# Kernel tuning notes

Measured on AMD Instinct MI355X. Metric: run time of the kernel, lower is better.

## Reference

```python
import jax, jax.numpy as jnp
import numpy as np

B, NPG, CIN, D, C, H, E, MAXN = 128, 1000, 16, 128, 12, 4, 640000, 1001
N = B * NPG
DH = D // H
NL = 3


def _ln(x, w, b):
    m = x.mean(-1, keepdims=True)
    v = ((x - m) ** 2).mean(-1, keepdims=True)
    return (x - m) * jax.lax.rsqrt(v + 1e-5) * w + b


def _mha(q_in, k_in, v_in, qkv_w, qkv_b, out_w, out_b, pad=None):
    # torch nn.MultiheadAttention with packed in_proj: rows [0:D]=Q, [D:2D]=K, [2D:3D]=V
    Tq, Tk = q_in.shape[1], k_in.shape[1]
    q = (q_in @ qkv_w[:D].T + qkv_b[:D]).reshape(-1, Tq, H, DH)
    k = (k_in @ qkv_w[D:2 * D].T + qkv_b[D:2 * D]).reshape(-1, Tk, H, DH)
    v = (v_in @ qkv_w[2 * D:].T + qkv_b[2 * D:]).reshape(-1, Tk, H, DH)
    s = jnp.einsum('bqhd,bkhd->bhqk', q, k) / np.sqrt(DH).astype(np.float32)
    if pad is not None:
        s = jnp.where(pad[:, None, None, :], jnp.float32(-1e30), s)
    a = jax.nn.softmax(s, axis=-1)
    o = jnp.einsum('bhqk,bkhd->bqhd', a, v).reshape(-1, Tq, D)
    return o @ out_w.T + out_b


def setup_inputs():
    key = jax.random.key(0)
    ks = iter(jax.random.split(key, 48))
    def nrm(shape, s=0.05):
        return jax.random.normal(next(ks), shape, jnp.float32) * s
    inp = {
        'x': nrm((N, CIN), 1.0),
        'edge_index': jax.random.randint(next(ks), (2, E), 0, N, dtype=jnp.int32),
        'batch': (jnp.arange(N, dtype=jnp.int32) // NPG),
        'in_w': nrm((D, CIN)), 'in_b': nrm((D,)),
        'gcn_w': nrm((NL, D, D)), 'gcn_b': nrm((NL, D)),
        'ln_w': jnp.ones((NL, D), jnp.float32), 'ln_b': jnp.zeros((NL, D), jnp.float32),
        'cq': nrm((C, D), 1.0),
        'sa_qkv_w': nrm((3 * D, D)), 'sa_qkv_b': nrm((3 * D,)),
        'sa_out_w': nrm((D, D)), 'sa_out_b': nrm((D,)),
        'ca_qkv_w': nrm((3 * D, D)), 'ca_qkv_b': nrm((3 * D,)),
        'ca_out_w': nrm((D, D)), 'ca_out_b': nrm((D,)),
        'n1_w': jnp.ones((D,), jnp.float32), 'n1_b': jnp.zeros((D,), jnp.float32),
        'n2_w': jnp.ones((D,), jnp.float32), 'n2_b': jnp.zeros((D,), jnp.float32),
        'n3_w': jnp.ones((D,), jnp.float32), 'n3_b': jnp.zeros((D,), jnp.float32),
        'ff1_w': nrm((4 * D, D)), 'ff1_b': nrm((4 * D,)),
        'ff2_w': nrm((D, 4 * D)), 'ff2_b': nrm((D,)),
        'op_ln_w': jnp.ones((D,), jnp.float32), 'op_ln_b': jnp.zeros((D,), jnp.float32),
        'op_w': nrm((1, D)), 'op_b': nrm((1,)),
    }
    return inp


def reference(x, edge_index, batch, in_w, in_b, gcn_w, gcn_b, ln_w, ln_b, cq,
              sa_qkv_w, sa_qkv_b, sa_out_w, sa_out_b,
              ca_qkv_w, ca_qkv_b, ca_out_w, ca_out_b,
              n1_w, n1_b, n2_w, n2_b, n3_w, n3_b,
              ff1_w, ff1_b, ff2_w, ff2_b, op_ln_w, op_ln_b, op_w, op_b):
    row, col = edge_index[0], edge_index[1]
    # ---- GCNBlock (eval mode: dropout = identity) ----
    h = x @ in_w.T + in_b  # input_proj since in_channels != hidden_dim
    # GCNConv normalization with self-loops (same for all layers)
    deg = jax.ops.segment_sum(jnp.ones((E,), h.dtype), col, num_segments=N) + 1.0
    dinv = jax.lax.rsqrt(deg)  # [N]
    en = dinv[row] * dinv[col]  # [E]
    self_w = (dinv * dinv)[:, None]
    residual = h
    for i in range(NL):
        hw = h @ gcn_w[i].T  # [N, D]
        agg = jax.ops.segment_sum(en[:, None] * hw[row], col, num_segments=N)
        agg = agg + self_w * hw + gcn_b[i]
        if i < NL - 1:
            h = jax.nn.relu(_ln(agg, ln_w[i], ln_b[i]))
            h = h + residual
            residual = h
        else:
            h = _ln(agg, ln_w[i], ln_b[i])
    # ---- pad variable-size graphs into dense memory + key padding mask ----
    counts = jax.ops.segment_sum(jnp.ones((N,), jnp.int32), batch, num_segments=B)
    starts = jnp.cumsum(counts) - counts
    pos = jnp.arange(N, dtype=jnp.int32) - starts[batch]
    memory = jnp.zeros((B, MAXN, D), h.dtype).at[batch, pos].set(h)
    pad = jnp.arange(MAXN)[None, :] >= counts[:, None]  # True = padded position
    # ---- TransformerDecoderLayer (norm_first=True), 1 layer ----
    t = jnp.broadcast_to(cq, (B, C, D))
    tn = _ln(t, n1_w, n1_b)
    t = t + _mha(tn, tn, tn, sa_qkv_w, sa_qkv_b, sa_out_w, sa_out_b)
    tn = _ln(t, n2_w, n2_b)
    t = t + _mha(tn, memory, memory, ca_qkv_w, ca_qkv_b, ca_out_w, ca_out_b, pad)
    tn = _ln(t, n3_w, n3_b)
    t = t + (jax.nn.relu(tn @ ff1_w.T + ff1_b) @ ff2_w.T + ff2_b)
    # ---- output projection: LN -> Linear(D,1) -> squeeze ----
    logits = (_ln(t, op_ln_w, op_ln_b) @ op_w.T + op_b)[..., 0]  # [B, C]
    return logits
```

## Files before the change

### kernel.cpp

```cpp
#include <hip/hip_runtime.h>
#include <hip/hip_bf16.h>

#define NNODES 128000
#define NEDGES 640000
#define BB 128
#define CC 12
#define DD 128
#define NROWS (BB*CC)
#define NSPLIT 8
#define CHUNK 125

typedef __attribute__((ext_vector_type(8))) short short8;
typedef __attribute__((ext_vector_type(4))) float f32x4;
typedef unsigned short ushort_t;

__device__ __forceinline__ unsigned pk2bf(float lo, float hi){
    union { __hip_bfloat162 h; unsigned u; } v;
    v.h = __float22bfloat162_rn(make_float2(lo, hi));
    return v.u;
}
__device__ __forceinline__ ushort_t f2bf(float f){
    union { __hip_bfloat16 h; ushort_t u; } v;
    v.h = __float2bfloat16(f);
    return v.u;
}
__device__ __forceinline__ float bfu_lo(unsigned u){
    union { unsigned u; float f; } v; v.u = u << 16; return v.f;
}
__device__ __forceinline__ float bfu_hi(unsigned u){
    union { unsigned u; float f; } v; v.u = u & 0xFFFF0000u; return v.f;
}

__global__ __launch_bounds__(256) void count_edges(const int* __restrict__ col, int* __restrict__ cnt){
    int e = blockIdx.x*256 + threadIdx.x;
    if (e < NEDGES) atomicAdd(&cnt[col[e]], 1);
}

__global__ __launch_bounds__(256) void scan_a(const int* __restrict__ cnt, int* __restrict__ offs,
        int* __restrict__ bsum, float* __restrict__ dinv){
    __shared__ int tmp[256];
    int tid = threadIdx.x;
    int g = blockIdx.x*256 + tid;
    int v = cnt[g];
    dinv[g] = rsqrtf((float)v + 1.0f);
    tmp[tid] = v;
    __syncthreads();
    for (int o=1;o<256;o<<=1){
        int a = (tid>=o)? tmp[tid-o] : 0;
        __syncthreads();
        tmp[tid] += a;
        __syncthreads();
    }
    offs[g] = tmp[tid] - v;
    if (tid==255) bsum[blockIdx.x] = tmp[255];
}

__global__ __launch_bounds__(512) void scan_b(int* __restrict__ bsum, int NB){
    __shared__ int tmp[512];
    int tid = threadIdx.x;
    int v = (tid<NB)? bsum[tid] : 0;
    tmp[tid] = v;
    __syncthreads();
    for (int o=1;o<512;o<<=1){
        int a = (tid>=o)? tmp[tid-o] : 0;
        __syncthreads();
        tmp[tid] += a;
        __syncthreads();
    }
    if (tid<NB) bsum[tid] = tmp[tid] - v;
}

__global__ __launch_bounds__(256) void scan_c(int* __restrict__ offs, const int* __restrict__ bsum){
    int g = blockIdx.x*256 + threadIdx.x;
    offs[g] += bsum[g>>8];
    if (g==0) offs[NNODES] = NEDGES;
}

__global__ __launch_bounds__(256) void fill_csr(const int* __restrict__ row, const int* __restrict__ col,
        const int* __restrict__ offs, int* __restrict__ cur, const float* __restrict__ dinv,
        int2* __restrict__ ee){
    int e = blockIdx.x*256 + threadIdx.x;
    if (e >= NEDGES) return;
    int c = col[e], r = row[e];
    int p = atomicAdd(&cur[c], 1);
    int idx = offs[c] + p;
    float w = dinv[r]*dinv[c];
    ee[idx] = make_int2(r, __float_as_int(w));
}

__global__ __launch_bounds__(256) void conv_all(const float* __restrict__ gcn_w,
        const float* __restrict__ ca_qkv_w, const float* __restrict__ in_w,
        const float* __restrict__ caout, const float* __restrict__ ff1, const float* __restrict__ ff2,
        ushort_t* __restrict__ Wb, ushort_t* __restrict__ Wpad, ushort_t* __restrict__ Wd){
    int i = blockIdx.x*256 + threadIdx.x;
    if (i < 81920){
        int slot = i >> 14, off = i & 16383;
        float v = (slot < 3) ? gcn_w[slot*16384 + off]
                             : ca_qkv_w[16384 + (slot-3)*16384 + off];
        Wb[i] = f2bf(v);
    } else if (i < 86016){
        int j = i - 81920;
        int n = j >> 5, k = j & 31;
        Wpad[j] = (k < 16) ? f2bf(in_w[n*16 + k]) : (ushort_t)0;
    } else {
        int j = i - 86016;
        float v;
        if (j < 16384) v = caout[j];
        else if (j < 81920) v = ff1[j - 16384];
        else v = ff2[j - 81920];
        Wd[j] = f2bf(v);
    }
}

__global__ __launch_bounds__(256) void in_proj_mfma(const float* __restrict__ x,
        const ushort_t* __restrict__ Wpad, const float* __restrict__ bias,
        ushort_t* __restrict__ hbf){
    __shared__ __align__(16) ushort_t xs[64*40];
    int tid = threadIdx.x;
    int m0 = blockIdx.x*64;
    if (tid < 128){
        short8 z = {0,0,0,0,0,0,0,0};
        *(short8*)&xs[(tid>>1)*40 + 16 + (tid&1)*8] = z;
    }
    float4 xv = *(const float4*)(x + (size_t)m0*16 + tid*4);
    uint2 pk2;
    pk2.x = pk2bf(xv.x, xv.y);
    pk2.y = pk2bf(xv.z, xv.w);
    *(uint2*)&xs[(tid>>2)*40 + (tid&3)*4] = pk2;
    __syncthreads();
    int lane = tid & 63, w = tid >> 6;
    int lr = lane & 15, hi4 = lane >> 4, lk = hi4*8;
    short8 wf[8];
    #pragma unroll
    for (int nt=0; nt<8; ++nt)
        wf[nt] = *(const short8*)&Wpad[(nt*16 + lr)*32 + lk];
    short8 a = *(const short8*)&xs[(w*16 + lr)*40 + lk];
    f32x4 acc[8];
    #pragma unroll
    for (int nt=0; nt<8; ++nt)
        acc[nt] = __builtin_amdgcn_mfma_f32_16x16x32_bf16(wf[nt], a, (f32x4){0,0,0,0}, 0, 0, 0);
    size_t m = (size_t)m0 + w*16 + lr;
    #pragma unroll
    for (int nt=0; nt<8; ++nt){
        int n0 = nt*16 + hi4*4;
        float4 bv = *(const float4*)&bias[n0];
        uint2 pk;
        pk.x = pk2bf(acc[nt][0]+bv.x, acc[nt][1]+bv.y);
        pk.y = pk2bf(acc[nt][2]+bv.z, acc[nt][3]+bv.w);
        *(uint2*)&hbf[m*128 + n0] = pk;
    }
}

__global__ __launch_bounds__(256) void gemm_mfma(const ushort_t* __restrict__ A,
        const ushort_t* __restrict__ Wb, const float* __restrict__ bias, ushort_t* __restrict__ out){
    __shared__ __align__(16) ushort_t wl[128*136];
    int tid = threadIdx.x;
    #pragma unroll
    for (int i=0;i<8;++i){
        int elem = tid*8 + i*2048;
        int row = elem >> 7, k = elem & 127;
        *(short8*)&wl[row*136 + k] = *(const short8*)&Wb[elem];
    }
    __syncthreads();
    int lane = tid & 63, wave = tid >> 6;
    int m0 = blockIdx.x*128 + wave*32;
    int lr = lane & 15, hi4 = lane >> 4;
    int lk = hi4 * 8;
    f32x4 acc[2][8];
    #pragma unroll
    for (int t=0;t<2;++t)
        #pragma unroll
        for (int nt=0;nt<8;++nt) acc[t][nt] = (f32x4){0.f,0.f,0.f,0.f};
    const ushort_t* arow0 = A + (size_t)(m0 + lr)*128 + lk;
    const ushort_t* arow1 = arow0 + 16*128;
    #pragma unroll
    for (int kc=0; kc<4; ++kc){
        short8 h0 = *(const short8*)(arow0 + kc*32);
        short8 h1 = *(const short8*)(arow1 + kc*32);
        #pragma unroll
        for (int nt=0; nt<8; ++nt){
            short8 wf = *(const short8*)&wl[(nt*16 + lr)*136 + kc*32 + lk];
            acc[0][nt] = __builtin_amdgcn_mfma_f32_16x16x32_bf16(wf, h0, acc[0][nt], 0, 0, 0);
            acc[1][nt] = __builtin_amdgcn_mfma_f32_16x16x32_bf16(wf, h1, acc[1][nt], 0, 0, 0);
        }
    }
    #pragma unroll
    for (int nt=0; nt<8; ++nt){
        int n0 = nt*16 + hi4*4;
        float b0=0.f,b1=0.f,b2=0.f,b3=0.f;
        if (bias){
            float4 bv = *(const float4*)&bias[n0];
            b0=bv.x; b1=bv.y; b2=bv.z; b3=bv.w;
        }
        #pragma unroll
        for (int t=0; t<2; ++t){
            size_t m = (size_t)m0 + t*16 + lr;
            uint2 pk;
            pk.x = pk2bf(acc[t][nt][0]+b0, acc[t][nt][1]+b1);
            pk.y = pk2bf(acc[t][nt][2]+b2, acc[t][nt][3]+b3);
            *(uint2*)&out[m*128 + n0] = pk;
        }
    }
}

__global__ __launch_bounds__(256) void gemm_mfma_kv(const ushort_t* __restrict__ A,
        const ushort_t* __restrict__ Wk, const ushort_t* __restrict__ Wv,
        const float* __restrict__ bk, const float* __restrict__ bv,
        ushort_t* __restrict__ outk, ushort_t* __restrict__ outv){
    __shared__ __align__(16) ushort_t wl[128*136];
    int tid = threadIdx.x;
    int lane = tid & 63, wave = tid >> 6;
    int m0 = blockIdx.x*128 + wave*32;
    int lr = lane & 15, hi4 = lane >> 4;
    int lk = hi4 * 8;
    const ushort_t* arow0 = A + (size_t)(m0 + lr)*128 + lk;
    const ushort_t* arow1 = arow0 + 16*128;
    short8 h0[4], h1[4];
    #pragma unroll
    for (int kc=0;kc<4;++kc){
        h0[kc] = *(const short8*)(arow0 + kc*32);
        h1[kc] = *(const short8*)(arow1 + kc*32);
    }
    #pragma unroll
    for (int i=0;i<8;++i){
        int elem = tid*8 + i*2048;
        int row = elem >> 7, k = elem & 127;
        *(short8*)&wl[row*136 + k] = *(const short8*)&Wk[elem];
    }
    __syncthreads();
    {
        f32x4 acc[2][8];
        #pragma unroll
        for (int t=0;t<2;++t)
            #pragma unroll
            for (int nt=0;nt<8;++nt) acc[t][nt] = (f32x4){0.f,0.f,0.f,0.f};
        #pragma unroll
        for (int kc=0; kc<4; ++kc){
            #pragma unroll
            for (int nt=0; nt<8; ++nt){
                short8 wf = *(const short8*)&wl[(nt*16 + lr)*136 + kc*32 + lk];
                acc[0][nt] = __builtin_amdgcn_mfma_f32_16x16x32_bf16(wf, h0[kc], acc[0][nt], 0, 0, 0);
                acc[1][nt] = __builtin_amdgcn_mfma_f32_16x16x32_bf16(wf, h1[kc], acc[1][nt], 0, 0, 0);
            }
        }
        #pragma unroll
        for (int nt=0; nt<8; ++nt){
            int n0 = nt*16 + hi4*4;
            float4 b4 = *(const float4*)&bk[n0];
            #pragma unroll
            for (int t=0; t<2; ++t){
                size_t m = (size_t)m0 + t*16 + lr;
                uint2 pk;
                pk.x = pk2bf(acc[t][nt][0]+b4.x, acc[t][nt][1]+b4.y);
                pk.y = pk2bf(acc[t][nt][2]+b4.z, acc[t][nt][3]+b4.w);
                *(uint2*)&outk[m*128 + n0] = pk;
            }
        }
    }
    __syncthreads();
    #pragma unroll
    for (int i=0;i<8;++i){
        int elem = tid*8 + i*2048;
        int row = elem >> 7, k = elem & 127;
        *(short8*)&wl[row*136 + k] = *(const short8*)&Wv[elem];
    }
    __syncthreads();
    {
        f32x4 acc[2][8];
        #pragma unroll
        for (int t=0;t<2;++t)
            #pragma unroll
            for (int nt=0;nt<8;++nt) acc[t][nt] = (f32x4){0.f,0.f,0.f,0.f};
        #pragma unroll
        for (int kc=0; kc<4; ++kc){
            #pragma unroll
            for (int nt=0; nt<8; ++nt){
                short8 wf = *(const short8*)&wl[(nt*16 + lr)*136 + kc*32 + lk];
                acc[0][nt] = __builtin_amdgcn_mfma_f32_16x16x32_bf16(wf, h0[kc], acc[0][nt], 0, 0, 0);
                acc[1][nt] = __builtin_amdgcn_mfma_f32_16x16x32_bf16(wf, h1[kc], acc[1][nt], 0, 0, 0);
            }
        }
        #pragma unroll
        for (int nt=0; nt<8; ++nt){
            int n0 = nt*16 + hi4*4;
            float4 b4 = *(const float4*)&bv[n0];
            #pragma unroll
            for (int t=0; t<2; ++t){
                size_t m = (size_t)m0 + t*16 + lr;
                uint2 pk;
                pk.x = pk2bf(acc[t][nt][0]+b4.x, acc[t][nt][1]+b4.y);
                pk.y = pk2bf(acc[t][nt][2]+b4.z, acc[t][nt][3]+b4.w);
                *(uint2*)&outv[m*128 + n0] = pk;
            }
        }
    }
}

__global__ __launch_bounds__(256) void gcn_agg(ushort_t* __restrict__ hbf, const ushort_t* __restrict__ hwbf,
        const int* __restrict__ offs, const int2* __restrict__ ee,
        const float* __restrict__ dinv, const float* __restrict__ bias,
        const float* __restrict__ lnw, const float* __restrict__ lnb, int last){
    int wave = threadIdx.x >> 6;
    int lane = threadIdx.x & 63;
    int g = lane >> 4, sl = lane & 15;
    int node = blockIdx.x*16 + wave*4 + g;
    const uint4* hwu = (const uint4*)hwbf;
    uint4* hbu = (uint4*)hbf;
    uint4 sv = hwu[(size_t)node*16 + sl];
    uint4 rv = make_uint4(0,0,0,0);
    if (!last) rv = hbu[(size_t)node*16 + sl];
    float di = dinv[node];
    float sw = di*di;
    float a0 = sw*bfu_lo(sv.x), a1 = sw*bfu_hi(sv.x);
    float a2 = sw*bfu_lo(sv.y), a3 = sw*bfu_hi(sv.y);
    float a4 = sw*bfu_lo(sv.z), a5 = sw*bfu_hi(sv.z);
    float a6 = sw*bfu_lo(sv.w), a7 = sw*bfu_hi(sv.w);
    float b0=0,b1=0,b2=0,b3=0,b4=0,b5=0,b6=0,b7=0;
    int e0 = offs[node], e1 = offs[node+1];
    int e = e0;
    for (; e + 4 <= e1; e += 4){
        int2 p0 = ee[e], p1 = ee[e+1], p2 = ee[e+2], p3 = ee[e+3];
        uint4 u0 = hwu[(size_t)p0.x*16 + sl];
        uint4 u1 = hwu[(size_t)p1.x*16 + sl];
        uint4 u2 = hwu[(size_t)p2.x*16 + sl];
        uint4 u3 = hwu[(size_t)p3.x*16 + sl];
        float w0 = __int_as_float(p0.y), w1 = __int_as_float(p1.y);
        float w2 = __int_as_float(p2.y), w3 = __int_as_float(p3.y);
        a0 += w0*bfu_lo(u0.x); a1 += w0*bfu_hi(u0.x); a2 += w0*bfu_lo(u0.y); a3 += w0*bfu_hi(u0.y);
        a4 += w0*bfu_lo(u0.z); a5 += w0*bfu_hi(u0.z); a6 += w0*bfu_lo(u0.w); a7 += w0*bfu_hi(u0.w);
        b0 += w1*bfu_lo(u1.x); b1 += w1*bfu_hi(u1.x); b2 += w1*bfu_lo(u1.y); b3 += w1*bfu_hi(u1.y);
        b4 += w1*bfu_lo(u1.z); b5 += w1*bfu_hi(u1.z); b6 += w1*bfu_lo(u1.w); b7 += w1*bfu_hi(u1.w);
        a0 += w2*bfu_lo(u2.x); a1 += w2*bfu_hi(u2.x); a2 += w2*bfu_lo(u2.y); a3 += w2*bfu_hi(u2.y);
        a4 += w2*bfu_lo(u2.z); a5 += w2*bfu_hi(u2.z); a6 += w2*bfu_lo(u2.w); a7 += w2*bfu_hi(u2.w);
        b0 += w3*bfu_lo(u3.x); b1 += w3*bfu_hi(u3.x); b2 += w3*bfu_lo(u3.y); b3 += w3*bfu_hi(u3.y);
        b4 += w3*bfu_lo(u3.z); b5 += w3*bfu_hi(u3.z); b6 += w3*bfu_lo(u3.w); b7 += w3*bfu_hi(u3.w);
    }
    if (e + 2 <= e1){
        int2 p0 = ee[e], p1 = ee[e+1];
        uint4 u0 = hwu[(size_t)p0.x*16 + sl];
        uint4 u1 = hwu[(size_t)p1.x*16 + sl];
        float w0 = __int_as_float(p0.y), w1 = __int_as_float(p1.y);
        a0 += w0*bfu_lo(u0.x); a1 += w0*bfu_hi(u0.x); a2 += w0*bfu_lo(u0.y); a3 += w0*bfu_hi(u0.y);
        a4 += w0*bfu_lo(u0.z); a5 += w0*bfu_hi(u0.z); a6 += w0*bfu_lo(u0.w); a7 += w0*bfu_hi(u0.w);
        b0 += w1*bfu_lo(u1.x); b1 += w1*bfu_hi(u1.x); b2 += w1*bfu_lo(u1.y); b3 += w1*bfu_hi(u1.y);
        b4 += w1*bfu_lo(u1.z); b5 += w1*bfu_hi(u1.z); b6 += w1*bfu_lo(u1.w); b7 += w1*bfu_hi(u1.w);
        e += 2;
    }
    if (e < e1){
        int2 p0 = ee[e];
        uint4 u0 = hwu[(size_t)p0.x*16 + sl];
        float w0 = __int_as_float(p0.y);
        a0 += w0*bfu_lo(u0.x); a1 += w0*bfu_hi(u0.x); a2 += w0*bfu_lo(u0.y); a3 += w0*bfu_hi(u0.y);
        a4 += w0*bfu_lo(u0.z); a5 += w0*bfu_hi(u0.z); a6 += w0*bfu_lo(u0.w); a7 += w0*bfu_hi(u0.w);
    }
    a0 += b0; a1 += b1; a2 += b2; a3 += b3;
    a4 += b4; a5 += b5; a6 += b6; a7 += b7;
    {
        const float4* b4p = (const float4*)bias;
        float4 bb0 = b4p[sl*2], bb1 = b4p[sl*2+1];
        a0 += bb0.x; a1 += bb0.y; a2 += bb0.z; a3 += bb0.w;
        a4 += bb1.x; a5 += bb1.y; a6 += bb1.z; a7 += bb1.w;
    }
    float s = ((a0+a1)+(a2+a3))+((a4+a5)+(a6+a7));
    s += __shfl_xor(s,1); s += __shfl_xor(s,2); s += __shfl_xor(s,4); s += __shfl_xor(s,8);
    float mean = s*(1.f/128.f);
    a0 -= mean; a1 -= mean; a2 -= mean; a3 -= mean;
    a4 -= mean; a5 -= mean; a6 -= mean; a7 -= mean;
    float var = ((a0*a0+a1*a1)+(a2*a2+a3*a3))+((a4*a4+a5*a5)+(a6*a6+a7*a7));
    var += __shfl_xor(var,1); var += __shfl_xor(var,2); var += __shfl_xor(var,4); var += __shfl_xor(var,8);
    float rs = rsqrtf(var*(1.f/128.f) + 1e-5f);
    float4 w0v = ((const float4*)lnw)[sl*2], w1v = ((const float4*)lnw)[sl*2+1];
    float4 l0v = ((const float4*)lnb)[sl*2], l1v = ((const float4*)lnb)[sl*2+1];
    float y0 = a0*rs*w0v.x + l0v.x;
    float y1 = a1*rs*w0v.y + l0v.y;
    float y2 = a2*rs*w0v.z + l0v.z;
    float y3 = a3*rs*w0v.w + l0v.w;
    float y4 = a4*rs*w1v.x + l1v.x;
    float y5 = a5*rs*w1v.y + l1v.y;
    float y6 = a6*rs*w1v.z + l1v.z;
    float y7 = a7*rs*w1v.w + l1v.w;
    if (!last){
        y0 = fmaxf(y0,0.f) + bfu_lo(rv.x);
        y1 = fmaxf(y1,0.f) + bfu_hi(rv.x);
        y2 = fmaxf(y2,0.f) + bfu_lo(rv.y);
        y3 = fmaxf(y3,0.f) + bfu_hi(rv.y);
        y4 = fmaxf(y4,0.f) + bfu_lo(rv.z);
        y5 = fmaxf(y5,0.f) + bfu_hi(rv.z);
        y6 = fmaxf(y6,0.f) + bfu_lo(rv.w);
        y7 = fmaxf(y7,0.f) + bfu_hi(rv.w);
    }
    uint4 pk;
    pk.x = pk2bf(y0, y1);
    pk.y = pk2bf(y2, y3);
    pk.z = pk2bf(y4, y5);
    pk.w = pk2bf(y6, y7);
    hbu[(size_t)node*16 + sl] = pk;
}

__global__ __launch_bounds__(256) void dec_gemm(const ushort_t* __restrict__ A,
        const ushort_t* __restrict__ Wb, const float* __restrict__ bias,
        float* __restrict__ out, ushort_t* __restrict__ outbf,
        const float* __restrict__ tbc,
        int K, int NO, int flags){
    int lane = threadIdx.x & 63, wave = threadIdx.x >> 6;
    int m0 = blockIdx.x*64 + wave*16;
    int n0 = blockIdx.y*128;
    int lr = lane & 15, lk = (lane>>4)*8;
    f32x4 acc[8];
    #pragma unroll
    for (int nt=0; nt<8; ++nt) acc[nt] = (f32x4){0.f,0.f,0.f,0.f};
    for (int ko = 0; ko < K; ko += 128){
        short8 bfrag[4][8];
        #pragma unroll
        for (int nt=0; nt<8; ++nt)
            #pragma unroll
            for (int kc=0; kc<4; ++kc)
                bfrag[kc][nt] = *(const short8*)&Wb[(size_t)(n0 + nt*16 + lr)*K + ko + kc*32 + lk];
        const ushort_t* arow = A + (size_t)(m0 + lr)*K + ko + lk;
        #pragma unroll
        for (int kc=0; kc<4; ++kc){
            short8 a = *(const short8*)(arow + kc*32);
            #pragma unroll
            for (int nt=0; nt<8; ++nt)
                acc[nt] = __builtin_amdgcn_mfma_f32_16x16x32_bf16(a, bfrag[kc][nt], acc[nt], 0, 0, 0);
        }
    }
    int orow0 = m0 + (lane>>4)*4;
    #pragma unroll
    for (int nt=0; nt<8; ++nt){
        int col = n0 + nt*16 + lr;
        float bv = bias[col];
        #pragma unroll
        for (int r=0; r<4; ++r){
            int row = orow0 + r;
            size_t idx = (size_t)row*NO + col;
            float val = acc[nt][r] + bv;
            if (flags & 2) val = fmaxf(val, 0.f);
            if (flags & 1) val += out[idx];
            if (flags & 16) val += tbc[(row % 12)*128 + col];
            if (flags & 8) out[idx] = val;
            if (flags & 4) outbf[idx] = f2bf(val);
        }
    }
}

__global__ __launch_bounds__(256) void ln_rows(const float* __restrict__ x, float* __restrict__ y,
        const float* __restrict__ w, const float* __restrict__ b){
    int r = blockIdx.x*4 + (threadIdx.x>>6);
    int lane = threadIdx.x & 63;
    const float2* x2 = (const float2*)(x + (size_t)r*128);
    float2 v = x2[lane];
    float s = v.x+v.y;
    for (int o=32;o>0;o>>=1) s += __shfl_xor(s,o);
    float mean = s*(1.f/128.f);
    float dx=v.x-mean, dy=v.y-mean;
    float var = dx*dx+dy*dy;
    for (int o=32;o>0;o>>=1) var += __shfl_xor(var,o);
    float rs = rsqrtf(var*(1.f/128.f) + 1e-5f);
    float2 w2=((const float2*)w)[lane], b2=((const float2*)b)[lane];
    ((float2*)(y + (size_t)r*128))[lane] = make_float2(dx*rs*w2.x+b2.x, dy*rs*w2.y+b2.y);
}

__global__ __launch_bounds__(256) void ln_rows_bf(const float* __restrict__ x, ushort_t* __restrict__ y,
        const float* __restrict__ w, const float* __restrict__ b){
    int r = blockIdx.x*4 + (threadIdx.x>>6);
    int lane = threadIdx.x & 63;
    const float2* x2 = (const float2*)(x + (size_t)r*128);
    float2 v = x2[lane];
    float s = v.x+v.y;
    for (int o=32;o>0;o>>=1) s += __shfl_xor(s,o);
    float mean = s*(1.f/128.f);
    float dx=v.x-mean, dy=v.y-mean;
    float var = dx*dx+dy*dy;
    for (int o=32;o>0;o>>=1) var += __shfl_xor(var,o);
    float rs = rsqrtf(var*(1.f/128.f) + 1e-5f);
    float2 w2=((const float2*)w)[lane], b2=((const float2*)b)[lane];
    float yx = dx*rs*w2.x+b2.x, yy = dy*rs*w2.y+b2.y;
    ((unsigned*)y)[(size_t)r*64 + lane] = pk2bf(yx, yy);
}

__global__ __launch_bounds__(256) void small_gemm(const float* __restrict__ x, const float* __restrict__ W,
        const float* __restrict__ bias, float* __restrict__ out, const float* __restrict__ base,
        int R, int K, int NO, int flags){
    int idx = blockIdx.x*256 + threadIdx.x;
    if (idx >= R*NO) return;
    int r = idx / NO, n = idx - r*NO;
    const float4* xr = (const float4*)(x + (size_t)r*K);
    const float4* wr = (const float4*)(W + (size_t)n*K);
    float a = bias ? bias[n] : 0.0f;
    int K4 = K>>2;
    for (int k=0;k<K4;++k){
        float4 xv = xr[k], wv = wr[k];
        a += xv.x*wv.x + xv.y*wv.y + xv.z*wv.z + xv.w*wv.w;
    }
    if (flags & 2) a = fmaxf(a, 0.f);
    if (flags & 1) a += out[idx];
    if (base) a += base[idx];
    out[idx] = a;
}

__global__ __launch_bounds__(64) void self_attn12(const float* __restrict__ qkv, float* __restrict__ out){
    int hh = blockIdx.x;
    int lane = threadIdx.x;
    __shared__ float q[12][32], k[12][32], v[12][32], sc[12][12];
    for (int idx = lane; idx < 12*32; idx += 64){
        int c = idx>>5, d = idx&31;
        size_t base = (size_t)c*384 + hh*32 + d;
        q[c][d] = qkv[base] * 0.17677669529663687f;
        k[c][d] = qkv[base+128];
        v[c][d] = qkv[base+256];
    }
    __syncthreads();
    for (int p = lane; p < 144; p += 64){
        int qi = p/12, ki = p%12;
        float a = 0;
        #pragma unroll
        for (int d=0; d<32; ++d) a += q[qi][d]*k[ki][d];
        sc[qi][ki] = a;
    }
    __syncthreads();
    if (lane < 12){
        float m = -1e30f;
        for (int j=0;j<12;++j) m = fmaxf(m, sc[lane][j]);
        float sum=0;
        for (int j=0;j<12;++j){ float e=__expf(sc[lane][j]-m); sc[lane][j]=e; sum+=e; }
        float inv=1.f/sum;
        for (int j=0;j<12;++j) sc[lane][j]*=inv;
    }
    __syncthreads();
    for (int p = lane; p < 384; p += 64){
        int c = p>>5, d = p&31;
        float a=0;
        #pragma unroll
        for (int j=0;j<12;++j) a += sc[c][j]*v[j][d];
        out[(size_t)c*128 + hh*32 + d] = a;
    }
}

__global__ __launch_bounds__(512) void cross_attn_part(const float* __restrict__ q12,
        const ushort_t* __restrict__ K, const ushort_t* __restrict__ V,
        float* __restrict__ opart, float2* __restrict__ mlpart){
    __shared__ __align__(16) ushort_t qs[16*136];
    __shared__ __align__(16) unsigned char uni[128*136*2];
    __shared__ __align__(16) ushort_t pbf[4*16*136];
    __shared__ float2 ml[48];
    float* s32 = (float*)uni;
    ushort_t* vt = (ushort_t*)uni;

    int tid = threadIdx.x;
    int b = blockIdx.x / NSPLIT, sp = blockIdx.x % NSPLIT;
    int k0 = sp * CHUNK;
    int lane = tid & 63, w = tid >> 6;
    int lr = lane & 15, hi8 = (lane >> 4) * 8;

    const unsigned* Vu = (const unsigned*)V + ((size_t)b*1000 + k0)*64;
    unsigned vreg[16];
    #pragma unroll
    for (int j=0;j<15;++j) vreg[j] = Vu[tid + j*512];
    if (tid < 320) vreg[15] = Vu[tid + 7680];

    for (int i = tid; i < 16*128; i += 512){
        int r = i >> 7, c = i & 127;
        ushort_t v = 0;
        if (r < 12) v = f2bf(q12[r*128 + c] * 0.17677669529663687f);
        qs[r*136 + c] = v;
    }
    for (int i = tid; i < 4352; i += 512) ((unsigned*)pbf)[i] = 0;
    __syncthreads();

    {
        int krow = k0 + w*16 + lr; if (krow > k0 + 124) krow = k0 + 124;
        const ushort_t* Krow = K + ((size_t)b*1000 + krow)*128 + hi8;
        #pragma unroll
        for (int h=0; h<4; ++h){
            short8 kf = *(const short8*)(Krow + h*32);
            short8 qf = *(const short8*)&qs[lr*136 + h*32 + hi8];
            f32x4 d = __builtin_amdgcn_mfma_f32_16x16x32_bf16(qf, kf, (f32x4){0,0,0,0}, 0, 0, 0);
            int qbase = (lane>>4)*4;
            #pragma unroll
            for (int r=0; r<4; ++r){
                int qq = qbase + r;
                if (qq < 12) s32[(h*12+qq)*130 + w*16 + lr] = d[r];
            }
        }
    }
    __syncthreads();

    if (tid < 192){
        int hq = tid >> 2, sub = tid & 3;
        int h = hq / 12, qq = hq - h*12;
        float m = -1e30f;
        for (int kk = sub; kk < CHUNK; kk += 4) m = fmaxf(m, s32[hq*130 + kk]);
        m = fmaxf(m, __shfl_xor(m, 1));
        m = fmaxf(m, __shfl_xor(m, 2));
        float l = 0.f;
        for (int kk = sub; kk < CHUNK; kk += 4){
            float e = __expf(s32[hq*130 + kk] - m);
            l += e;
            pbf[(h*16+qq)*136 + kk] = f2bf(e);
        }
        l += __shfl_xor(l, 1);
        l += __shfl_xor(l, 2);
        if (sub == 0) ml[hq] = make_float2(m, l);
    }
    __syncthreads();

    #pragma unroll
    for (int j=0;j<15;++j){
        int i = tid + j*512;
        int kk = i >> 6, dp = (i & 63)*2;
        unsigned u = vreg[j];
        vt[dp*136 + kk]     = (ushort_t)(u & 0xFFFF);
        vt[(dp+1)*136 + kk] = (ushort_t)(u >> 16);
    }
    if (tid < 320){
        int i = tid + 7680;
        int kk = i >> 6, dp = (i & 63)*2;
        unsigned u = vreg[15];
        vt[dp*136 + kk]     = (ushort_t)(u & 0xFFFF);
        vt[(dp+1)*136 + kk] = (ushort_t)(u >> 16);
    }
    if (tid < 384){
        int dp = tid / 3, kk = 125 + tid % 3;
        vt[dp*136 + kk] = 0;
    }
    __syncthreads();

    {
        int h = w >> 1;
        f32x4 acc = (f32x4){0,0,0,0};
        #pragma unroll
        for (int kc=0; kc<4; ++kc){
            short8 pf = *(const short8*)&pbf[(h*16+lr)*136 + kc*32 + hi8];
            short8 vf = *(const short8*)&vt[(w*16+lr)*136 + kc*32 + hi8];
            acc = __builtin_amdgcn_mfma_f32_16x16x32_bf16(pf, vf, acc, 0, 0, 0);
        }
        int qbase = (lane>>4)*4;
        float* ob = opart + ((size_t)(b*NSPLIT+sp)*12)*128;
        #pragma unroll
        for (int r=0; r<4; ++r){
            int qq = qbase + r;
            if (qq < 12) ob[(size_t)qq*128 + w*16 + lr] = acc[r];
        }
    }
    if (tid < 48) mlpart[(size_t)(b*NSPLIT+sp)*48 + tid] = ml[tid];
}

__global__ __launch_bounds__(256) void cross_attn_comb(const float* __restrict__ opart,
        const float* __restrict__ mlpart, ushort_t* __restrict__ attbf){
    int b = blockIdx.x, tid = threadIdx.x;
    __shared__ float mls[NSPLIT*48*2];
    for (int i = tid; i < NSPLIT*48*2; i += 256) mls[i] = mlpart[(size_t)b*NSPLIT*96 + i];
    __syncthreads();
    for (int p = tid; p < 1536; p += 256){
        int qq = p >> 7, dp = p & 127, h = dp >> 5, hq = h*12 + qq;
        float M = -1e30f;
        #pragma unroll
        for (int sp=0; sp<NSPLIT; ++sp) M = fmaxf(M, mls[sp*96 + hq*2]);
        float L = 0.f, O = 0.f;
        #pragma unroll
        for (int sp=0; sp<NSPLIT; ++sp){
            float wgt = __expf(mls[sp*96 + hq*2] - M);
            L += wgt * mls[sp*96 + hq*2 + 1];
            O += wgt * opart[((size_t)(b*NSPLIT+sp)*12 + qq)*128 + dp];
        }
        attbf[((size_t)b*12 + qq)*128 + dp] = f2bf(O / L);
    }
}

__global__ __launch_bounds__(256) void final_out(const float* __restrict__ t,
        const float* __restrict__ lw, const float* __restrict__ lb,
        const float* __restrict__ ow, const float* __restrict__ ob, float* __restrict__ out){
    int r = blockIdx.x*4 + (threadIdx.x>>6);
    int lane = threadIdx.x & 63;
    const float2* x2 = (const float2*)(t + (size_t)r*128);
    float2 v = x2[lane];
    float s = v.x+v.y;
    for (int o=32;o>0;o>>=1) s += __shfl_xor(s,o);
    float mean = s*(1.f/128.f);
    float dx=v.x-mean, dy=v.y-mean;
    float var = dx*dx+dy*dy;
    for (int o=32;o>0;o>>=1) var += __shfl_xor(var,o);
    float rs = rsqrtf(var*(1.f/128.f)+1e-5f);
    float2 w2=((const float2*)lw)[lane], b2=((const float2*)lb)[lane];
    float2 o2=((const float2*)ow)[lane];
    float d = (dx*rs*w2.x+b2.x)*o2.x + (dy*rs*w2.y+b2.y)*o2.y;
    for (int o=32;o>0;o>>=1) d += __shfl_xor(d,o);
    if (lane==0) out[r] = d + ob[0];
}

extern "C" void kernel_launch(void* const* d_in, const int* in_sizes, int n_in,
                              void* d_out, int out_size, void* d_ws, size_t ws_size,
                              hipStream_t stream){
    (void)in_sizes; (void)n_in; (void)out_size; (void)ws_size;
    const float* x        = (const float*)d_in[0];
    const int*   eidx     = (const int*)d_in[1];
    const float* in_w     = (const float*)d_in[3];
    const float* in_b     = (const float*)d_in[4];
    const float* gcn_w    = (const float*)d_in[5];
    const float* gcn_b    = (const float*)d_in[6];
    const float* ln_w     = (const float*)d_in[7];
    const float* ln_b     = (const float*)d_in[8];
    const float* cq       = (const float*)d_in[9];
    const float* sa_qkv_w = (const float*)d_in[10];
    const float* sa_qkv_b = (const float*)d_in[11];
    const float* sa_out_w = (const float*)d_in[12];
    const float* sa_out_b = (const float*)d_in[13];
    const float* ca_qkv_w = (const float*)d_in[14];
    const float* ca_qkv_b = (const float*)d_in[15];
    const float* ca_out_w = (const float*)d_in[16];
    const float* ca_out_b = (const float*)d_in[17];
    const float* n1w=(const float*)d_in[18]; const float* n1b=(const float*)d_in[19];
    const float* n2w=(const float*)d_in[20]; const float* n2b=(const float*)d_in[21];
    const float* n3w=(const float*)d_in[22]; const float* n3b=(const float*)d_in[23];
    const float* ff1w=(const float*)d_in[24]; const float* ff1b=(const float*)d_in[25];
    const float* ff2w=(const float*)d_in[26]; const float* ff2b=(const float*)d_in[27];
    const float* opln_w=(const float*)d_in[28]; const float* opln_b=(const float*)d_in[29];
    const float* opw=(const float*)d_in[30]; const float* opb=(const float*)d_in[31];
    float* out = (float*)d_out;

    char* base = (char*)d_ws;
    size_t off = 0;
    auto alloc = [&](size_t bytes)->void*{
        void* r = base + off; off += (bytes + 255) & ~(size_t)255; return r;
    };
    ushort_t* hbf   = (ushort_t*)alloc((size_t)NNODES*DD*2);
    ushort_t* kbf   = (ushort_t*)alloc((size_t)NNODES*DD*2);
    ushort_t* vbf   = (ushort_t*)alloc((size_t)NNODES*DD*2);
    ushort_t* Wb    = (ushort_t*)alloc((size_t)5*DD*DD*2);
    ushort_t* Wpad  = (ushort_t*)alloc((size_t)DD*32*2);
    ushort_t* Wdec  = (ushort_t*)alloc((size_t)147456*2);
    float*    dinv  = (float*)alloc((size_t)NNODES*4);
    int*      cnt   = (int*)  alloc((size_t)NNODES*4);
    int*      offs  = (int*)  alloc((size_t)(NNODES+1)*4);
    int*      bsum  = (int*)  alloc(512*4);
    int2*     ee    = (int2*) alloc((size_t)NEDGES*8);
    float*    t12   = (float*)alloc((size_t)12*DD*4);
    float*    tn12  = (float*)alloc((size_t)12*DD*4);
    float*    sq12  = (float*)alloc((size_t)12*384*4);
    float*    att12 = (float*)alloc((size_t)12*DD*4);
    float*    q12   = (float*)alloc((size_t)12*DD*4);
    float*    tfull = (float*)alloc((size_t)NROWS*DD*4);
    ushort_t* tnbf  = (ushort_t*)alloc((size_t)NROWS*DD*2);
    ushort_t* attbf = (ushort_t*)alloc((size_t)NROWS*DD*2);
    ushort_t* ffhbf = (ushort_t*)alloc((size_t)NROWS*512*2);
    float*    opart = (float*)alloc((size_t)BB*NSPLIT*12*128*4);
    float2*   mlprt = (float2*)alloc((size_t)BB*NSPLIT*48*8);
    ushort_t* hwbf  = kbf;

    const int* erow = eidx;
    const int* ecol = eidx + NEDGES;

    hipMemsetAsync(cnt, 0, (size_t)NNODES*4, stream);
    count_edges<<<NEDGES/256, 256, 0, stream>>>(ecol, cnt);
    scan_a<<<NNODES/256, 256, 0, stream>>>(cnt, offs, bsum, dinv);
    scan_b<<<1, 512, 0, stream>>>(bsum, NNODES/256);
    scan_c<<<NNODES/256, 256, 0, stream>>>(offs, bsum);
    hipMemsetAsync(cnt, 0, (size_t)NNODES*4, stream);
    fill_csr<<<NEDGES/256, 256, 0, stream>>>(erow, ecol, offs, cnt, dinv, ee);

    conv_all<<<912, 256, 0, stream>>>(gcn_w, ca_qkv_w, in_w, ca_out_w, ff1w, ff2w, Wb, Wpad, Wdec);

    in_proj_mfma<<<NNODES/64, 256, 0, stream>>>(x, Wpad, in_b, hbf);
    for (int i=0;i<3;++i){
        gemm_mfma<<<NNODES/128, 256, 0, stream>>>(hbf, Wb + (size_t)i*DD*DD, nullptr, hwbf);
        gcn_agg<<<NNODES/16, 256, 0, stream>>>(hbf, hwbf, offs, ee, dinv,
                gcn_b + (size_t)i*DD, ln_w + (size_t)i*DD, ln_b + (size_t)i*DD, i==2);
    }
    gemm_mfma_kv<<<NNODES/128, 256, 0, stream>>>(hbf, Wb + (size_t)3*DD*DD, Wb + (size_t)4*DD*DD,
            ca_qkv_b + DD, ca_qkv_b + 2*DD, kbf, vbf);

    ln_rows<<<3, 256, 0, stream>>>(cq, tn12, n1w, n1b);
    small_gemm<<<18, 256, 0, stream>>>(tn12, sa_qkv_w, sa_qkv_b, sq12, nullptr, 12, 128, 384, 0);
    self_attn12<<<4, 64, 0, stream>>>(sq12, att12);
    small_gemm<<<6, 256, 0, stream>>>(att12, sa_out_w, sa_out_b, t12, cq, 12, 128, 128, 0);
    ln_rows<<<3, 256, 0, stream>>>(t12, tn12, n2w, n2b);
    small_gemm<<<6, 256, 0, stream>>>(tn12, ca_qkv_w, ca_qkv_b, q12, nullptr, 12, 128, 128, 0);

    cross_attn_part<<<BB*NSPLIT, 512, 0, stream>>>(q12, kbf, vbf, opart, mlprt);
    cross_attn_comb<<<BB, 256, 0, stream>>>(opart, (const float*)mlprt, attbf);
    dim3 g24_1(24,1), g24_4(24,4);
    dec_gemm<<<g24_1, 256, 0, stream>>>(attbf, Wdec, ca_out_b, tfull, nullptr, t12, 128, 128, 16|8);
    ln_rows_bf<<<NROWS/4, 256, 0, stream>>>(tfull, tnbf, n3w, n3b);
    dec_gemm<<<g24_4, 256, 0, stream>>>(tnbf, Wdec + 16384, ff1b, nullptr, ffhbf, nullptr, 128, 512, 2|4);
    dec_gemm<<<g24_1, 256, 0, stream>>>(ffhbf, Wdec + 81920, ff2b, tfull, nullptr, nullptr, 512, 128, 1|8);
    final_out<<<NROWS/4, 256, 0, stream>>>(tfull, opln_w, opln_b, opw, opb, out);
}
```

Measured before the change: 421.4 us.

## Halve GEMM row tile and stage weights in two LDS halves

The node GEMM kernels now process 64 rows per block (16 per wave) instead of 128, doubling the grid. The weight matrix is staged through shared memory in two 64-row halves with padding 132, cutting LDS from about 34KB to about 17KB, and accumulators drop from 16 to 8 vectors. The goal is higher occupancy and more blocks to hide load latency. In exchange the weights are reloaded twice as often across blocks, and each block adds extra barriers.

```diff
diff --git a/kernel.cpp b/kernel.cpp
--- a/kernel.cpp
+++ b/kernel.cpp
@@ -153,53 +153,51 @@
 
 __global__ __launch_bounds__(256) void gemm_mfma(const ushort_t* __restrict__ A,
         const ushort_t* __restrict__ Wb, const float* __restrict__ bias, ushort_t* __restrict__ out){
-    __shared__ __align__(16) ushort_t wl[128*136];
+    __shared__ __align__(16) ushort_t wl[64*132];
     int tid = threadIdx.x;
-    #pragma unroll
-    for (int i=0;i<8;++i){
-        int elem = tid*8 + i*2048;
-        int row = elem >> 7, k = elem & 127;
-        *(short8*)&wl[row*136 + k] = *(const short8*)&Wb[elem];
-    }
-    __syncthreads();
     int lane = tid & 63, wave = tid >> 6;
-    int m0 = blockIdx.x*128 + wave*32;
+    int m0 = blockIdx.x*64 + wave*16;
     int lr = lane & 15, hi4 = lane >> 4;
     int lk = hi4 * 8;
-    f32x4 acc[2][8];
-    #pragma unroll
-    for (int t=0;t<2;++t)
-        #pragma unroll
-        for (int nt=0;nt<8;++nt) acc[t][nt] = (f32x4){0.f,0.f,0.f,0.f};
-    const ushort_t* arow0 = A + (size_t)(m0 + lr)*128 + lk;
-    const ushort_t* arow1 = arow0 + 16*128;
-    #pragma unroll
-    for (int kc=0; kc<4; ++kc){
-        short8 h0 = *(const short8*)(arow0 + kc*32);
-        short8 h1 = *(const short8*)(arow1 + kc*32);
-        #pragma unroll
-        for (int nt=0; nt<8; ++nt){
-            short8 wf = *(const short8*)&wl[(nt*16 + lr)*136 + kc*32 + lk];
-            acc[0][nt] = __builtin_amdgcn_mfma_f32_16x16x32_bf16(wf, h0, acc[0][nt], 0, 0, 0);
-            acc[1][nt] = __builtin_amdgcn_mfma_f32_16x16x32_bf16(wf, h1, acc[1][nt], 0, 0, 0);
-        }
-    }
-    #pragma unroll
-    for (int nt=0; nt<8; ++nt){
-        int n0 = nt*16 + hi4*4;
+    const ushort_t* arow = A + (size_t)(m0 + lr)*128 + lk;
+    short8 h[4];
+    #pragma unroll
+    for (int kc=0;kc<4;++kc) h[kc] = *(const short8*)(arow + kc*32);
+    f32x4 acc[8];
+    #pragma unroll
+    for (int j=0;j<8;++j) acc[j] = (f32x4){0.f,0.f,0.f,0.f};
+    #pragma unroll
+    for (int ph=0; ph<2; ++ph){
+        if (ph) __syncthreads();
+        #pragma unroll
+        for (int i=0;i<4;++i){
+            int e = tid*8 + i*2048;
+            int row = e >> 7, k = e & 127;
+            *(short8*)&wl[row*132 + k] = *(const short8*)&Wb[(ph*64 + row)*128 + k];
+        }
+        __syncthreads();
+        #pragma unroll
+        for (int kc=0; kc<4; ++kc){
+            #pragma unroll
+            for (int nt=0; nt<4; ++nt){
+                short8 wf = *(const short8*)&wl[(nt*16 + lr)*132 + kc*32 + lk];
+                acc[ph*4+nt] = __builtin_amdgcn_mfma_f32_16x16x32_bf16(wf, h[kc], acc[ph*4+nt], 0, 0, 0);
+            }
+        }
+    }
+    size_t m = (size_t)m0 + lr;
+    #pragma unroll
+    for (int j=0; j<8; ++j){
+        int n0 = j*16 + hi4*4;
         float b0=0.f,b1=0.f,b2=0.f,b3=0.f;
         if (bias){
             float4 bv = *(const float4*)&bias[n0];
             b0=bv.x; b1=bv.y; b2=bv.z; b3=bv.w;
         }
-        #pragma unroll
-        for (int t=0; t<2; ++t){
-            size_t m = (size_t)m0 + t*16 + lr;
-            uint2 pk;
-            pk.x = pk2bf(acc[t][nt][0]+b0, acc[t][nt][1]+b1);
-            pk.y = pk2bf(acc[t][nt][2]+b2, acc[t][nt][3]+b3);
-            *(uint2*)&out[m*128 + n0] = pk;
-        }
+        uint2 pk;
+        pk.x = pk2bf(acc[j][0]+b0, acc[j][1]+b1);
+        pk.y = pk2bf(acc[j][2]+b2, acc[j][3]+b3);
+        *(uint2*)&out[m*128 + n0] = pk;
     }
 }
 
@@ -207,92 +205,77 @@
         const ushort_t* __restrict__ Wk, const ushort_t* __restrict__ Wv,
         const float* __restrict__ bk, const float* __restrict__ bv,
         ushort_t* __restrict__ outk, ushort_t* __restrict__ outv){
-    __shared__ __align__(16) ushort_t wl[128*136];
+    __shared__ __align__(16) ushort_t wl[64*132];
     int tid = threadIdx.x;
     int lane = tid & 63, wave = tid >> 6;
-    int m0 = blockIdx.x*128 + wave*32;
+    int m0 = blockIdx.x*64 + wave*16;
     int lr = lane & 15, hi4 = lane >> 4;
     int lk = hi4 * 8;
-    const ushort_t* arow0 = A + (size_t)(m0 + lr)*128 + lk;
-    const ushort_t* arow1 = arow0 + 16*128;
-    short8 h0[4], h1[4];
-    #pragma unroll
-    for (int kc=0;kc<4;++kc){
-        h0[kc] = *(const short8*)(arow0 + kc*32);
-        h1[kc] = *(const short8*)(arow1 + kc*32);
-    }
-    #pragma unroll
-    for (int i=0;i<8;++i){
-        int elem = tid*8 + i*2048;
-        int row = elem >> 7, k = elem & 127;
-        *(short8*)&wl[row*136 + k] = *(const short8*)&Wk[elem];
-    }
-    __syncthreads();
-    {
-        f32x4 acc[2][8];
-        #pragma unroll
-        for (int t=0;t<2;++t)
-            #pragma unroll
-            for (int nt=0;nt<8;++nt) acc[t][nt] = (f32x4){0.f,0.f,0.f,0.f};
+    const ushort_t* arow = A + (size_t)(m0 + lr)*128 + lk;
+    short8 h[4];
+    #pragma unroll
+    for (int kc=0;kc<4;++kc) h[kc] = *(const short8*)(arow + kc*32);
+    size_t m = (size_t)m0 + lr;
+    f32x4 acc[8];
+    #pragma unroll
+    for (int j=0;j<8;++j) acc[j] = (f32x4){0.f,0.f,0.f,0.f};
+    #pragma unroll
+    for (int ph=0; ph<2; ++ph){
+        if (ph) __syncthreads();
+        #pragma unroll
+        for (int i=0;i<4;++i){
+            int e = tid*8 + i*2048;
+            int row = e >> 7, k = e & 127;
+            *(short8*)&wl[row*132 + k] = *(const short8*)&Wk[(ph*64 + row)*128 + k];
+        }
+        __syncthreads();
         #pragma unroll
         for (int kc=0; kc<4; ++kc){
             #pragma unroll
-            for (int nt=0; nt<8; ++nt){
-                short8 wf = *(const short8*)&wl[(nt*16 + lr)*136 + kc*32 + lk];
-                acc[0][nt] = __builtin_amdgcn_mfma_f32_16x16x32_bf16(wf, h0[kc], acc[0][nt], 0, 0, 0);
-                acc[1][nt] = __builtin_amdgcn_mfma_f32_16x16x32_bf16(wf, h1[kc], acc[1][nt], 0, 0, 0);
+            for (int nt=0; nt<4; ++nt){
+                short8 wf = *(const short8*)&wl[(nt*16 + lr)*132 + kc*32 + lk];
+                acc[ph*4+nt] = __builtin_amdgcn_mfma_f32_16x16x32_bf16(wf, h[kc], acc[ph*4+nt], 0, 0, 0);
             }
         }
-        #pragma unroll
-        for (int nt=0; nt<8; ++nt){
-            int n0 = nt*16 + hi4*4;
-            float4 b4 = *(const float4*)&bk[n0];
-            #pragma unroll
-            for (int t=0; t<2; ++t){
-                size_t m = (size_t)m0 + t*16 + lr;
-                uint2 pk;
-                pk.x = pk2bf(acc[t][nt][0]+b4.x, acc[t][nt][1]+b4.y);
-                pk.y = pk2bf(acc[t][nt][2]+b4.z, acc[t][nt][3]+b4.w);
-                *(uint2*)&outk[m*128 + n0] = pk;
-            }
-        }
-    }
-    __syncthreads();
-    #pragma unroll
-    for (int i=0;i<8;++i){
-        int elem = tid*8 + i*2048;
-        int row = elem >> 7, k = elem & 127;
-        *(short8*)&wl[row*136 + k] = *(const short8*)&Wv[elem];
-    }
-    __syncthreads();
-    {
-        f32x4 acc[2][8];
-        #pragma unroll
-        for (int t=0;t<2;++t)
-            #pragma unroll
-            for (int nt=0;nt<8;++nt) acc[t][nt] = (f32x4){0.f,0.f,0.f,0.f};
+    }
+    #pragma unroll
+    for (int j=0; j<8; ++j){
+        int n0 = j*16 + hi4*4;
+        float4 bv4 = *(const float4*)&bk[n0];
+        uint2 pk;
+        pk.x = pk2bf(acc[j][0]+bv4.x, acc[j][1]+bv4.y);
+        pk.y = pk2bf(acc[j][2]+bv4.z, acc[j][3]+bv4.w);
+        *(uint2*)&outk[m*128 + n0] = pk;
+    }
+    #pragma unroll
+    for (int j=0;j<8;++j) acc[j] = (f32x4){0.f,0.f,0.f,0.f};
+    #pragma unroll
+    for (int ph=0; ph<2; ++ph){
+        __syncthreads();
+        #pragma unroll
+        for (int i=0;i<4;++i){
+            int e = tid*8 + i*2048;
+            int row = e >> 7, k = e & 127;
+            *(short8*)&wl[row*132 + k] = *(const short8*)&Wv[(ph*64 + row)*128 + k];
+        }
+        __syncthreads();
         #pragma unroll
         for (int kc=0; kc<4; ++kc){
             #pragma unroll
-            for (int nt=0; nt<8; ++nt){
-                short8 wf = *(const short8*)&wl[(nt*16 + lr)*136 + kc*32 + lk];
-                acc[0][nt] = __builtin_amdgcn_mfma_f32_16x16x32_bf16(wf, h0[kc], acc[0][nt], 0, 0, 0);
-                acc[1][nt] = __builtin_amdgcn_mfma_f32_16x16x32_bf16(wf, h1[kc], acc[1][nt], 0, 0, 0);
+            for (int nt=0; nt<4; ++nt){
+                short8 wf = *(const short8*)&wl[(nt*16 + lr)*132 + kc*32 + lk];
+                acc[ph*4+nt] = __builtin_amdgcn_mfma_f32_16x16x32_bf16(wf, h[kc], acc[ph*4+nt], 0, 0, 0);
             }
         }
-        #pragma unroll
-        for (int nt=0; nt<8; ++nt){
-            int n0 = nt*16 + hi4*4;
-            float4 b4 = *(const float4*)&bv[n0];
-            #pragma unroll
-            for (int t=0; t<2; ++t){
-                size_t m = (size_t)m0 + t*16 + lr;
-                uint2 pk;
-                pk.x = pk2bf(acc[t][nt][0]+b4.x, acc[t][nt][1]+b4.y);
-                pk.y = pk2bf(acc[t][nt][2]+b4.z, acc[t][nt][3]+b4.w);
-                *(uint2*)&outv[m*128 + n0] = pk;
-            }
-        }
+    }
+    #pragma unroll
+    for (int j=0; j<8; ++j){
+        int n0 = j*16 + hi4*4;
+        float4 bv4 = *(const float4*)&bv[n0];
+        uint2 pk;
+        pk.x = pk2bf(acc[j][0]+bv4.x, acc[j][1]+bv4.y);
+        pk.y = pk2bf(acc[j][2]+bv4.z, acc[j][3]+bv4.w);
+        *(uint2*)&outv[m*128 + n0] = pk;
     }
 }
 
@@ -763,11 +746,11 @@
 
     in_proj_mfma<<<NNODES/64, 256, 0, stream>>>(x, Wpad, in_b, hbf);
     for (int i=0;i<3;++i){
-        gemm_mfma<<<NNODES/128, 256, 0, stream>>>(hbf, Wb + (size_t)i*DD*DD, nullptr, hwbf);
+        gemm_mfma<<<NNODES/64, 256, 0, stream>>>(hbf, Wb + (size_t)i*DD*DD, nullptr, hwbf);
         gcn_agg<<<NNODES/16, 256, 0, stream>>>(hbf, hwbf, offs, ee, dinv,
                 gcn_b + (size_t)i*DD, ln_w + (size_t)i*DD, ln_b + (size_t)i*DD, i==2);
     }
-    gemm_mfma_kv<<<NNODES/128, 256, 0, stream>>>(hbf, Wb + (size_t)3*DD*DD, Wb + (size_t)4*DD*DD,
+    gemm_mfma_kv<<<NNODES/64, 256, 0, stream>>>(hbf, Wb + (size_t)3*DD*DD, Wb + (size_t)4*DD*DD,
             ca_qkv_b + DD, ca_qkv_b + 2*DD, kbf, vbf);
 
     ln_rows<<<3, 256, 0, stream>>>(cq, tn12, n1w, n1b);
```

Result: no change. 413.9 us (-1.8%).
